# Optimization experiments

Measured on AMD Instinct MI355X. Metric: run time of the kernel, lower is better.

The kernel has to match this reference:

```python
import jax, jax.numpy as jnp
import numpy as np

N = 200000      # number of nodes (src == dst, homogeneous graph)
E = 3200000     # number of edges (avg degree 16)
IN_FEATS = 256
N_CLASSES = 32


def setup_inputs() -> dict:
    key = jax.random.key(0)
    k = jax.random.split(key, 7)
    x = jax.random.normal(k[0], (N, IN_FEATS), dtype=jnp.float32)
    w = jax.random.uniform(k[1], (E,), dtype=jnp.float32)
    u_sum = jax.random.uniform(k[2], (N,), dtype=jnp.float32)
    W_weight = jax.random.normal(k[3], (N_CLASSES, IN_FEATS), dtype=jnp.float32) * (1.0 / np.sqrt(IN_FEATS))
    W_bias = jax.random.normal(k[4], (N_CLASSES,), dtype=jnp.float32) * 0.01
    src = jax.random.randint(k[5], (E,), 0, N, dtype=jnp.int32)
    dst = jax.random.randint(k[6], (E,), 0, N, dtype=jnp.int32)
    return {"x": x, "w": w, "u_sum": u_sum, "W_weight": W_weight,
            "W_bias": W_bias, "src": src, "dst": dst}


def reference(x, w, u_sum, W_weight, W_bias, src, dst):
    # Linear projection: h = x @ W^T + b -> [N, C]
    h = jnp.einsum('nf,cf->nc', x, W_weight) + W_bias
    # u_mul_e: message m = h[src] * w (per-edge scalar weight), then scatter-sum to dst
    msg = h[src] * w[:, None]                              # [E, C]
    y = jax.ops.segment_sum(msg, dst, num_segments=N)      # [N, C]
    # regularization loss
    mean_x = jnp.mean(y, axis=0)                           # [C]
    mean_u = u_sum / N                                     # [N]
    diff = mean_u[:, None] * h - mean_x                    # [N, C]
    reg_loss = jnp.sum(diff * diff) / (N * N_CLASSES)
    return (y, reg_loss)
```

## Files before the change

kernel.cpp:

```cpp
#include <hip/hip_runtime.h>
#include <hip/hip_bf16.h>

#define N_NODES 200000
#define N_EDGES 3200000
#define FEATS   256
#define NC      32

#define NBPB    128
#define BUCKETS 1563
#define CAP     2560

#define TILE_E  6144
#define NBK     521

typedef __attribute__((ext_vector_type(8))) short bf16x8;
typedef __attribute__((ext_vector_type(4))) float f32x4;

__device__ __forceinline__ float atomAddF(float* p, float v) {
    return unsafeAtomicAdd(p, v);
}
__device__ __forceinline__ short f2bf(float f) {
    return (short)__bfloat16_as_ushort(__float2bfloat16(f));
}

__global__ __launch_bounds__(256) void k_init(float* acc, int* pos)
{
    int i = blockIdx.x * 256 + threadIdx.x;
    if (i < 256) acc[i] = 0.f;
    if (i < BUCKETS) pos[i] = i * CAP;
}

__global__ __launch_bounds__(256, 3) void k_linear(
    const float* __restrict__ x, const float* __restrict__ Wmat,
    const float* __restrict__ bias, const float* __restrict__ u_sum,
    ushort* __restrict__ h_bf, float* __restrict__ S1, float* __restrict__ S2)
{
    __shared__ float lds_s1[4][32];
    __shared__ float lds_s2[4];

    const int lane = threadIdx.x & 63;
    const int wv   = threadIdx.x >> 6;
    const int lr   = lane & 15;
    const int kc   = lane >> 4;

    bf16x8 bfr[8][2];
    #pragma unroll
    for (int ct = 0; ct < 2; ++ct) {
        const float* wp = Wmat + (size_t)(ct * 16 + lr) * FEATS + kc * 8;
        #pragma unroll
        for (int kt = 0; kt < 8; ++kt) {
            f32x4 v0 = *(const f32x4*)(wp + kt * 32);
            f32x4 v1 = *(const f32x4*)(wp + kt * 32 + 4);
            bf16x8 b;
            b[0]=f2bf(v0.x); b[1]=f2bf(v0.y); b[2]=f2bf(v0.z); b[3]=f2bf(v0.w);
            b[4]=f2bf(v1.x); b[5]=f2bf(v1.y); b[6]=f2bf(v1.z); b[7]=f2bf(v1.w);
            bfr[kt][ct] = b;
        }
    }

    const float bias0 = bias[lr], bias1 = bias[16 + lr];
    const float invn = 1.0f / (float)N_NODES;
    float s1_0 = 0.f, s1_1 = 0.f, s2 = 0.f;

    const int ntiles = N_NODES / 16;
    for (int t = blockIdx.x * 4 + wv; t < ntiles; t += gridDim.x * 4) {
        const int base = t * 16;
        const float* xp = x + (size_t)(base + lr) * FEATS + kc * 8;
        f32x4 acc0 = {bias0, bias0, bias0, bias0};
        f32x4 acc1 = {bias1, bias1, bias1, bias1};
        #pragma unroll
        for (int kt = 0; kt < 8; ++kt) {
            f32x4 v0 = *(const f32x4*)(xp + kt * 32);
            f32x4 v1 = *(const f32x4*)(xp + kt * 32 + 4);
            bf16x8 a;
            a[0]=f2bf(v0.x); a[1]=f2bf(v0.y); a[2]=f2bf(v0.z); a[3]=f2bf(v0.w);
            a[4]=f2bf(v1.x); a[5]=f2bf(v1.y); a[6]=f2bf(v1.z); a[7]=f2bf(v1.w);
            acc0 = __builtin_amdgcn_mfma_f32_16x16x32_bf16(a, bfr[kt][0], acc0, 0, 0, 0);
            acc1 = __builtin_amdgcn_mfma_f32_16x16x32_bf16(a, bfr[kt][1], acc1, 0, 0, 0);
        }
        #pragma unroll
        for (int i = 0; i < 4; ++i) {
            const int row = base + kc * 4 + i;
            h_bf[(size_t)row * NC + lr]      = (ushort)f2bf(acc0[i]);
            h_bf[(size_t)row * NC + 16 + lr] = (ushort)f2bf(acc1[i]);
            const float um = u_sum[row] * invn;
            float a0 = um * acc0[i], a1 = um * acc1[i];
            s1_0 += a0; s1_1 += a1;
            s2 += a0 * a0 + a1 * a1;
        }
    }

    s1_0 += __shfl_xor(s1_0, 16); s1_0 += __shfl_xor(s1_0, 32);
    s1_1 += __shfl_xor(s1_1, 16); s1_1 += __shfl_xor(s1_1, 32);
    #pragma unroll
    for (int off = 1; off < 64; off <<= 1) s2 += __shfl_xor(s2, off);
    if (lane < 16) { lds_s1[wv][lr] = s1_0; lds_s1[wv][16 + lr] = s1_1; }
    if (lane == 0) lds_s2[wv] = s2;
    __syncthreads();
    if (threadIdx.x < 32) {
        float t4 = lds_s1[0][threadIdx.x] + lds_s1[1][threadIdx.x]
                 + lds_s1[2][threadIdx.x] + lds_s1[3][threadIdx.x];
        atomAddF(&S1[threadIdx.x], t4);
    }
    if (threadIdx.x == 32)
        atomAddF(S2, lds_s2[0] + lds_s2[1] + lds_s2[2] + lds_s2[3]);
}

__global__ __launch_bounds__(512, 2) void k_bucket(
    const int* __restrict__ src, const float* __restrict__ w,
    const int* __restrict__ dst, int* __restrict__ pos,
    int2* __restrict__ bucketed)
{
    __shared__ int2 eSort[TILE_E];
    __shared__ uint hist[2048];
    __shared__ int  scur[2048];
    __shared__ int  delta[2048];
    __shared__ int  tsum[512];

    const int tid = threadIdx.x;
    for (int i = tid; i < 2048; i += 512) hist[i] = 0u;
    __syncthreads();

    const int E4 = N_EDGES / 4;
    const int t4 = blockIdx.x * (TILE_E / 4);
    int4 dd[3];
    #pragma unroll
    for (int i = 0; i < 3; ++i) {
        int e4 = t4 + i * 512 + tid;
        if (e4 < E4) {
            int4 d = ((const int4*)dst)[e4];
            dd[i] = d;
            atomicAdd(&hist[d.x >> 7], 1u);
            atomicAdd(&hist[d.y >> 7], 1u);
            atomicAdd(&hist[d.z >> 7], 1u);
            atomicAdd(&hist[d.w >> 7], 1u);
        } else dd[i].x = -1;
    }
    __syncthreads();

    const int h0 = (int)hist[tid * 4 + 0], h1 = (int)hist[tid * 4 + 1];
    const int h2 = (int)hist[tid * 4 + 2], h3 = (int)hist[tid * 4 + 3];
    const int lsum = h0 + h1 + h2 + h3;
    tsum[tid] = lsum;
    __syncthreads();
    for (int off = 1; off < 512; off <<= 1) {
        int v = (tid >= off) ? tsum[tid - off] : 0;
        __syncthreads();
        tsum[tid] += v;
        __syncthreads();
    }
    const int texcl = tsum[tid] - lsum;
    scur[tid * 4 + 0] = texcl;
    scur[tid * 4 + 1] = texcl + h0;
    scur[tid * 4 + 2] = texcl + h0 + h1;
    scur[tid * 4 + 3] = texcl + h0 + h1 + h2;
    __syncthreads();

    for (int b = tid; b < BUCKETS; b += 512) {
        int hc = (int)hist[b];
        int g  = hc ? atomicAdd(&pos[b], hc) : 0;
        delta[b] = g - scur[b];
    }
    __syncthreads();

    #pragma unroll
    for (int i = 0; i < 3; ++i) {
        if (dd[i].x >= 0) {
            int e4 = t4 + i * 512 + tid;
            int4   s4 = ((const int4*)src)[e4];
            float4 w4 = ((const float4*)w)[e4];
            int d, q; int2 v;
            d = dd[i].x; q = atomicAdd(&scur[d >> 7], 1);
            v.x = s4.x | ((d & 127) << 18); v.y = __float_as_int(w4.x); eSort[q] = v;
            d = dd[i].y; q = atomicAdd(&scur[d >> 7], 1);
            v.x = s4.y | ((d & 127) << 18); v.y = __float_as_int(w4.y); eSort[q] = v;
            d = dd[i].z; q = atomicAdd(&scur[d >> 7], 1);
            v.x = s4.z | ((d & 127) << 18); v.y = __float_as_int(w4.z); eSort[q] = v;
            d = dd[i].w; q = atomicAdd(&scur[d >> 7], 1);
            v.x = s4.w | ((d & 127) << 18); v.y = __float_as_int(w4.w); eSort[q] = v;
        }
    }
    __syncthreads();

    int nblk = N_EDGES - blockIdx.x * TILE_E;
    if (nblk > TILE_E) nblk = TILE_E;
    for (int i = tid; i < nblk; i += 512) {
        int lo = 0, hi = BUCKETS - 1;
        while (lo < hi) {
            int mid = (lo + hi) >> 1;
            if (scur[mid] > i) hi = mid; else lo = mid + 1;
        }
        int2 v = eSort[i];
        bucketed[i + delta[lo]] = v;
    }
}

__global__ __launch_bounds__(512) void k_breduce(
    const int2* __restrict__ bucketed, const int* __restrict__ pos,
    const ushort* __restrict__ h_bf,
    float* __restrict__ y, float* __restrict__ colsum)
{
    __shared__ int2  eSort[CAP];
    __shared__ int   scnt[NBPB];
    __shared__ int   soffs[NBPB];
    __shared__ int   scur[NBPB];
    __shared__ int   ssc[NBPB];
    __shared__ float red[512];

    const int tid = threadIdx.x;
    const int b   = blockIdx.x;
    const int beg = b * CAP;
    const int n   = pos[b] - beg;

    if (tid < NBPB) scnt[tid] = 0;
    __syncthreads();

    int2 pr0, pr1, pr2, pr3, pr4;
    int  l0 = -1, l1 = -1, l2 = -1, l3 = -1, l4 = -1;
    if (tid          < n) { pr0 = bucketed[beg + tid];          l0 = (unsigned)pr0.x >> 18; }
    if (tid +  512   < n) { pr1 = bucketed[beg + tid + 512];    l1 = (unsigned)pr1.x >> 18; }
    if (tid + 1024   < n) { pr2 = bucketed[beg + tid + 1024];   l2 = (unsigned)pr2.x >> 18; }
    if (tid + 1536   < n) { pr3 = bucketed[beg + tid + 1536];   l3 = (unsigned)pr3.x >> 18; }
    if (tid + 2048   < n) { pr4 = bucketed[beg + tid + 2048];   l4 = (unsigned)pr4.x >> 18; }
    if (l0 >= 0) atomicAdd(&scnt[l0], 1);
    if (l1 >= 0) atomicAdd(&scnt[l1], 1);
    if (l2 >= 0) atomicAdd(&scnt[l2], 1);
    if (l3 >= 0) atomicAdd(&scnt[l3], 1);
    if (l4 >= 0) atomicAdd(&scnt[l4], 1);
    __syncthreads();

    if (tid < NBPB) ssc[tid] = scnt[tid];
    __syncthreads();
    for (int off = 1; off < NBPB; off <<= 1) {
        int t = 0;
        if (tid < NBPB && tid >= off) t = ssc[tid - off];
        __syncthreads();
        if (tid < NBPB && tid >= off) ssc[tid] += t;
        __syncthreads();
    }
    if (tid < NBPB) {
        int o = ssc[tid] - scnt[tid];
        soffs[tid] = o;
        scur[tid]  = o;
    }
    __syncthreads();

    if (l0 >= 0) { int q = atomicAdd(&scur[l0], 1); eSort[q] = pr0; }
    if (l1 >= 0) { int q = atomicAdd(&scur[l1], 1); eSort[q] = pr1; }
    if (l2 >= 0) { int q = atomicAdd(&scur[l2], 1); eSort[q] = pr2; }
    if (l3 >= 0) { int q = atomicAdd(&scur[l3], 1); eSort[q] = pr3; }
    if (l4 >= 0) { int q = atomicAdd(&scur[l4], 1); eSort[q] = pr4; }
    __syncthreads();

    const __hip_bfloat16* hb = (const __hip_bfloat16*)h_bf;
    const int c = tid & 31;
    const int g = tid >> 5;
    float scol = 0.f;
    for (int ld = g; ld < NBPB; ld += 16) {
        const int node = b * NBPB + ld;
        if (node >= N_NODES) break;
        int j = soffs[ld];
        const int e = j + scnt[ld];
        float s = 0.f;
        for (; j + 4 <= e; j += 4) {
            int2 p0 = eSort[j], p1 = eSort[j + 1], p2 = eSort[j + 2], p3 = eSort[j + 3];
            float h0 = __bfloat162float(hb[(size_t)(p0.x & 0x3FFFF) * NC + c]);
            float h1 = __bfloat162float(hb[(size_t)(p1.x & 0x3FFFF) * NC + c]);
            float h2 = __bfloat162float(hb[(size_t)(p2.x & 0x3FFFF) * NC + c]);
            float h3 = __bfloat162float(hb[(size_t)(p3.x & 0x3FFFF) * NC + c]);
            s = fmaf(h0, __int_as_float(p0.y), s);
            s = fmaf(h1, __int_as_float(p1.y), s);
            s = fmaf(h2, __int_as_float(p2.y), s);
            s = fmaf(h3, __int_as_float(p3.y), s);
        }
        for (; j < e; ++j) {
            int2 p = eSort[j];
            float hv = __bfloat162float(hb[(size_t)(p.x & 0x3FFFF) * NC + c]);
            s = fmaf(hv, __int_as_float(p.y), s);
        }
        y[(size_t)node * NC + c] = s;
        scol += s;
    }

    red[tid] = scol;
    __syncthreads();
    if (tid < 32) {
        float t = 0.f;
        #pragma unroll
        for (int jj = 0; jj < 16; ++jj) t += red[tid + 32 * jj];
        atomAddF(&colsum[tid], t);
    }
}

__global__ __launch_bounds__(256) void k_scatter_atomic(
    const ushort* __restrict__ h_bf, const float* __restrict__ w,
    const int* __restrict__ src, const int* __restrict__ dst,
    float* __restrict__ y)
{
    const __hip_bfloat16* hb = (const __hip_bfloat16*)h_bf;
    const long long total  = (long long)N_EDGES * NC;
    const long long stride = (long long)gridDim.x * 256;
    for (long long i = (long long)blockIdx.x * 256 + threadIdx.x;
         i < total; i += stride) {
        const int e = (int)(i >> 5);
        const int c = (int)(i & 31);
        float hv = __bfloat162float(hb[(size_t)src[e] * NC + c]);
        atomAddF(&y[(size_t)dst[e] * NC + c], hv * w[e]);
    }
}

__global__ __launch_bounds__(256) void k_colsum(
    const float* __restrict__ y, float* __restrict__ colsum)
{
    __shared__ float red[256];
    const long long total  = (long long)N_NODES * NC;
    const long long stride = (long long)gridDim.x * 256;
    float s = 0.f;
    for (long long i = (long long)blockIdx.x * 256 + threadIdx.x;
         i < total; i += stride)
        s += y[i];
    red[threadIdx.x] = s;
    __syncthreads();
    if (threadIdx.x < 32) {
        float t = 0.f;
        #pragma unroll
        for (int j = 0; j < 8; ++j) t += red[threadIdx.x + 32 * j];
        atomAddF(&colsum[threadIdx.x], t);
    }
}

__global__ void k_final(const float* __restrict__ acc, float* __restrict__ loss_out)
{
    double cross = 0.0, msq = 0.0;
    for (int c = 0; c < NC; ++c) {
        double m = (double)acc[c] / (double)N_NODES;
        cross += m * (double)acc[32 + c];
        msq   += m * m;
    }
    double loss = ((double)acc[64] - 2.0 * cross + (double)N_NODES * msq)
                  / ((double)N_NODES * (double)NC);
    *loss_out = (float)loss;
}

extern "C" void kernel_launch(void* const* d_in, const int* in_sizes, int n_in,
                              void* d_out, int out_size, void* d_ws, size_t ws_size,
                              hipStream_t stream)
{
    const float* x   = (const float*)d_in[0];
    const float* w   = (const float*)d_in[1];
    const float* u   = (const float*)d_in[2];
    const float* Wm  = (const float*)d_in[3];
    const float* Wb  = (const float*)d_in[4];
    const int*   src = (const int*)d_in[5];
    const int*   dst = (const int*)d_in[6];

    float* out = (float*)d_out;

    uint8_t* w8 = (uint8_t*)d_ws;
    float*  acc  = (float*)w8;
    int*    pos  = (int*)(w8 + 1024);
    ushort* h_bf = (ushort*)(w8 + 1024 + 8192);
    int2*   bucketed = (int2*)(w8 + 1024 + 8192 + (size_t)N_NODES * NC * 2);

    const size_t need = 1024 + 8192 + (size_t)N_NODES * NC * 2
                      + (size_t)BUCKETS * CAP * 8;

    if (ws_size >= need) {
        k_init   <<<8, 256, 0, stream>>>(acc, pos);
        k_linear <<<1024, 256, 0, stream>>>(x, Wm, Wb, u, h_bf, acc + 32, acc + 64);
        k_bucket <<<NBK, 512, 0, stream>>>(src, w, dst, pos, bucketed);
        k_breduce<<<BUCKETS, 512, 0, stream>>>(bucketed, pos, h_bf, out, acc);
    } else {
        k_init<<<8, 256, 0, stream>>>(acc, pos);
        hipMemsetAsync(d_out, 0, (size_t)out_size * sizeof(float), stream);
        k_linear        <<<1024, 256, 0, stream>>>(x, Wm, Wb, u, h_bf, acc + 32, acc + 64);
        k_scatter_atomic<<<8192, 256, 0, stream>>>(h_bf, w, src, dst, out);
        k_colsum        <<<2048, 256, 0, stream>>>(out, acc);
    }

    k_final<<<1, 1, 0, stream>>>(acc, out + (size_t)N_NODES * NC);
}
```

Measured before the change: 197.8 us.

## Scatter bucketed edges directly to global memory, dropping the in-LDS sort stage

The bucketing kernel no longer sorts each tile in LDS with a prefix scan and binary search. Each block builds a histogram, reserves global slots per bucket with one atomic, then writes every edge straight to its global position using LDS cursors. Counts now start at zero through a memset that replaces the init kernel, and the reduce kernel clamps counts to CAP. This removes the scan, the LDS staging buffer and several barriers, but the global writes become scattered rather than coalesced. The linear kernel's grid is also doubled, which is a separate launch-size change.

```diff
diff --git a/kernel.cpp b/kernel.cpp
--- a/kernel.cpp
+++ b/kernel.cpp
@@ -10,9 +10,6 @@
 #define BUCKETS 1563
 #define CAP     2560
 
-#define TILE_E  6144
-#define NBK     521
-
 typedef __attribute__((ext_vector_type(8))) short bf16x8;
 typedef __attribute__((ext_vector_type(4))) float f32x4;
 
@@ -21,13 +18,6 @@
 }
 __device__ __forceinline__ short f2bf(float f) {
     return (short)__bfloat16_as_ushort(__float2bfloat16(f));
-}
-
-__global__ __launch_bounds__(256) void k_init(float* acc, int* pos)
-{
-    int i = blockIdx.x * 256 + threadIdx.x;
-    if (i < 256) acc[i] = 0.f;
-    if (i < BUCKETS) pos[i] = i * CAP;
 }
 
 __global__ __launch_bounds__(256, 3) void k_linear(
@@ -106,92 +96,58 @@
         atomAddF(S2, lds_s2[0] + lds_s2[1] + lds_s2[2] + lds_s2[3]);
 }
 
-__global__ __launch_bounds__(512, 2) void k_bucket(
+__global__ __launch_bounds__(1024, 8) void k_bucket(
     const int* __restrict__ src, const float* __restrict__ w,
     const int* __restrict__ dst, int* __restrict__ pos,
     int2* __restrict__ bucketed)
 {
-    __shared__ int2 eSort[TILE_E];
-    __shared__ uint hist[2048];
-    __shared__ int  scur[2048];
-    __shared__ int  delta[2048];
-    __shared__ int  tsum[512];
-
+    __shared__ int hist[BUCKETS];
+    __shared__ int cursor[BUCKETS];
     const int tid = threadIdx.x;
-    for (int i = tid; i < 2048; i += 512) hist[i] = 0u;
+    for (int i = tid; i < BUCKETS; i += 1024) hist[i] = 0;
     __syncthreads();
 
     const int E4 = N_EDGES / 4;
-    const int t4 = blockIdx.x * (TILE_E / 4);
-    int4 dd[3];
+    const int t4 = blockIdx.x * 2048;
+    int4 dd[2];
     #pragma unroll
-    for (int i = 0; i < 3; ++i) {
-        int e4 = t4 + i * 512 + tid;
+    for (int i = 0; i < 2; ++i) {
+        int e4 = t4 + i * 1024 + tid;
         if (e4 < E4) {
             int4 d = ((const int4*)dst)[e4];
             dd[i] = d;
-            atomicAdd(&hist[d.x >> 7], 1u);
-            atomicAdd(&hist[d.y >> 7], 1u);
-            atomicAdd(&hist[d.z >> 7], 1u);
-            atomicAdd(&hist[d.w >> 7], 1u);
+            atomicAdd(&hist[d.x >> 7], 1);
+            atomicAdd(&hist[d.y >> 7], 1);
+            atomicAdd(&hist[d.z >> 7], 1);
+            atomicAdd(&hist[d.w >> 7], 1);
         } else dd[i].x = -1;
     }
     __syncthreads();
-
-    const int h0 = (int)hist[tid * 4 + 0], h1 = (int)hist[tid * 4 + 1];
-    const int h2 = (int)hist[tid * 4 + 2], h3 = (int)hist[tid * 4 + 3];
-    const int lsum = h0 + h1 + h2 + h3;
-    tsum[tid] = lsum;
-    __syncthreads();
-    for (int off = 1; off < 512; off <<= 1) {
-        int v = (tid >= off) ? tsum[tid - off] : 0;
-        __syncthreads();
-        tsum[tid] += v;
-        __syncthreads();
-    }
-    const int texcl = tsum[tid] - lsum;
-    scur[tid * 4 + 0] = texcl;
-    scur[tid * 4 + 1] = texcl + h0;
-    scur[tid * 4 + 2] = texcl + h0 + h1;
-    scur[tid * 4 + 3] = texcl + h0 + h1 + h2;
-    __syncthreads();
-
-    for (int b = tid; b < BUCKETS; b += 512) {
-        int hc = (int)hist[b];
-        int g  = hc ? atomicAdd(&pos[b], hc) : 0;
-        delta[b] = g - scur[b];
-    }
-    __syncthreads();
-
+    for (int i = tid; i < BUCKETS; i += 1024) {
+        int hc = hist[i];
+        cursor[i] = hc ? (i * CAP + atomicAdd(&pos[i], hc)) : 0;
+    }
+    __syncthreads();
     #pragma unroll
-    for (int i = 0; i < 3; ++i) {
+    for (int i = 0; i < 2; ++i) {
+        int e4 = t4 + i * 1024 + tid;
         if (dd[i].x >= 0) {
-            int e4 = t4 + i * 512 + tid;
             int4   s4 = ((const int4*)src)[e4];
             float4 w4 = ((const float4*)w)[e4];
             int d, q; int2 v;
-            d = dd[i].x; q = atomicAdd(&scur[d >> 7], 1);
-            v.x = s4.x | ((d & 127) << 18); v.y = __float_as_int(w4.x); eSort[q] = v;
-            d = dd[i].y; q = atomicAdd(&scur[d >> 7], 1);
-            v.x = s4.y | ((d & 127) << 18); v.y = __float_as_int(w4.y); eSort[q] = v;
-            d = dd[i].z; q = atomicAdd(&scur[d >> 7], 1);
-            v.x = s4.z | ((d & 127) << 18); v.y = __float_as_int(w4.z); eSort[q] = v;
-            d = dd[i].w; q = atomicAdd(&scur[d >> 7], 1);
-            v.x = s4.w | ((d & 127) << 18); v.y = __float_as_int(w4.w); eSort[q] = v;
-        }
-    }
-    __syncthreads();
-
-    int nblk = N_EDGES - blockIdx.x * TILE_E;
-    if (nblk > TILE_E) nblk = TILE_E;
-    for (int i = tid; i < nblk; i += 512) {
-        int lo = 0, hi = BUCKETS - 1;
-        while (lo < hi) {
-            int mid = (lo + hi) >> 1;
-            if (scur[mid] > i) hi = mid; else lo = mid + 1;
-        }
-        int2 v = eSort[i];
-        bucketed[i + delta[lo]] = v;
+            d = dd[i].x; q = atomicAdd(&cursor[d >> 7], 1);
+            v.x = s4.x | ((d & 127) << 18); v.y = __float_as_int(w4.x);
+            bucketed[q] = v;
+            d = dd[i].y; q = atomicAdd(&cursor[d >> 7], 1);
+            v.x = s4.y | ((d & 127) << 18); v.y = __float_as_int(w4.y);
+            bucketed[q] = v;
+            d = dd[i].z; q = atomicAdd(&cursor[d >> 7], 1);
+            v.x = s4.z | ((d & 127) << 18); v.y = __float_as_int(w4.z);
+            bucketed[q] = v;
+            d = dd[i].w; q = atomicAdd(&cursor[d >> 7], 1);
+            v.x = s4.w | ((d & 127) << 18); v.y = __float_as_int(w4.w);
+            bucketed[q] = v;
+        }
     }
 }
 
@@ -210,7 +166,8 @@
     const int tid = threadIdx.x;
     const int b   = blockIdx.x;
     const int beg = b * CAP;
-    const int n   = pos[b] - beg;
+    int n = pos[b];
+    if (n > CAP) n = CAP;
 
     if (tid < NBPB) scnt[tid] = 0;
     __syncthreads();
@@ -365,15 +322,15 @@
     const size_t need = 1024 + 8192 + (size_t)N_NODES * NC * 2
                       + (size_t)BUCKETS * CAP * 8;
 
+    hipMemsetAsync(w8, 0, 1024 + 8192, stream);
+
     if (ws_size >= need) {
-        k_init   <<<8, 256, 0, stream>>>(acc, pos);
-        k_linear <<<1024, 256, 0, stream>>>(x, Wm, Wb, u, h_bf, acc + 32, acc + 64);
-        k_bucket <<<NBK, 512, 0, stream>>>(src, w, dst, pos, bucketed);
+        k_linear <<<2048, 256, 0, stream>>>(x, Wm, Wb, u, h_bf, acc + 32, acc + 64);
+        k_bucket <<<391, 1024, 0, stream>>>(src, w, dst, pos, bucketed);
         k_breduce<<<BUCKETS, 512, 0, stream>>>(bucketed, pos, h_bf, out, acc);
     } else {
-        k_init<<<8, 256, 0, stream>>>(acc, pos);
         hipMemsetAsync(d_out, 0, (size_t)out_size * sizeof(float), stream);
-        k_linear        <<<1024, 256, 0, stream>>>(x, Wm, Wb, u, h_bf, acc + 32, acc + 64);
+        k_linear        <<<2048, 256, 0, stream>>>(x, Wm, Wb, u, h_bf, acc + 32, acc + 64);
         k_scatter_atomic<<<8192, 256, 0, stream>>>(h_bf, w, src, dst, out);
         k_colsum        <<<2048, 256, 0, stream>>>(out, acc);
     }
```

New measurement: 222.1 us. 1.12x slower.
